# Kernel tuning notes

Hardware: AMD Instinct MI355X
Metric: run time of the kernel (lower is better)

The kernel has to match this reference:

```python
import jax, jax.numpy as jnp
import numpy as np

# Cleaned/faithful JAX port of TATLMPLayer. The original torch code has obvious
# typos (edge_type_feature_embedding used before assignment, self.weight_mlp vs
# self._weight_mlp, missing dim= in concatenate, elementwise mult of (B,E,K) with
# (K,D)); we implement the clearly intended math: two-level masked-softmax
# message passing over an incidence matrix H, gumbel-softmax typed edge
# embeddings, and a 4-head cross-attention to polyline features.

NEG_SLOPE = 0.01  # torch leaky_relu default
TAU = 0.5         # gumbel-softmax temperature 1/2


def _mlp(x, W1, b1, W2, b2):
    return jnp.maximum(x @ W1 + b1, 0.0) @ W2 + b2


def setup_inputs() -> dict:
    B, N, E, P, D, T, K, Hd = 2, 256, 512, 256, 128, 8, 8, 256
    key = jax.random.key(0)
    ks = jax.random.split(key, 40)
    g = lambda i, shape, s=0.05: jax.random.normal(ks[i], shape, dtype=jnp.float32) * s
    return {
        "agent_features": jax.random.normal(ks[0], (B, N, D), dtype=jnp.float32),
        "agent_types": jax.random.uniform(ks[1], (B, N, T), dtype=jnp.float32),
        "polyline_features": jax.random.normal(ks[2], (B, P, D), dtype=jnp.float32),
        "H": (jax.random.uniform(ks[3], (B, E, N)) < 0.1).astype(jnp.float32),
        "type_emb": g(4, (K, D)),
        "w_W1": g(5, (2 * D, Hd)), "w_b1": g(6, (Hd,)), "w_W2": g(7, (Hd, 1)), "w_b2": g(8, (1,)),
        "d_W1": g(9, (D + T, Hd)), "d_b1": g(10, (Hd,)), "d_W2": g(11, (Hd, K)), "d_b2": g(12, (K,)),
        "f_W1": g(13, (D + T, Hd)), "f_b1": g(14, (Hd,)), "f_W2": g(15, (Hd, 1)), "f_b2": g(16, (1,)),
        "o_W1": g(17, (4 * D, Hd)), "o_b1": g(18, (Hd,)), "o_W2": g(19, (Hd, D)), "o_b2": g(20, (D,)),
        "q_W": g(21, (3 * D, D)), "q_b": g(22, (D,)),
        "k_W": g(23, (D, D)), "k_b": g(24, (D,)),
        "v_W": g(25, (D, D)), "v_b": g(26, (D,)),
        "iq_W": g(27, (D, D)), "iq_b": g(28, (D,)),
        "ik_W": g(29, (D, D)), "ik_b": g(30, (D,)),
        "iv_W": g(31, (D, D)), "iv_b": g(32, (D,)),
        "op_W": g(33, (D, D)), "op_b": g(34, (D,)),
    }


def reference(agent_features, agent_types, polyline_features, H, type_emb,
              w_W1, w_b1, w_W2, w_b2, d_W1, d_b1, d_W2, d_b2,
              f_W1, f_b1, f_W2, f_b2, o_W1, o_b1, o_W2, o_b2,
              q_W, q_b, k_W, k_b, v_W, v_b,
              iq_W, iq_b, ik_W, ik_b, iv_W, iv_b, op_W, op_b):
    B, N, D = agent_features.shape
    E = H.shape[1]

    # level 1: incidence-aggregated edge features
    ef_init = jnp.einsum('ben,bnd->bed', H, agent_features)            # (B,E,D)
    pair = jnp.concatenate([
        jnp.broadcast_to(ef_init[:, :, None, :], (B, E, N, D)),
        jnp.broadcast_to(agent_features[:, None, :, :], (B, E, N, D))], axis=-1)
    ew = _mlp(pair, w_W1, w_b1, w_W2, w_b2)[..., 0]                    # (B,E,N)
    Hw = jax.nn.softmax(ew * H, axis=2) * H
    edge_features = jnp.einsum('ben,bnd->bed', Hw, agent_features)     # (B,E,D)

    # typed edge embedding via gumbel-softmax over edge types
    edge_type = jnp.einsum('ben,bnt->bet', H, agent_types)             # (B,E,T)
    et = jnp.concatenate([edge_features, edge_type], axis=-1)          # (B,E,D+T)
    logits = _mlp(et, d_W1, d_b1, d_W2, d_b2)                          # (B,E,K)
    u = jax.random.uniform(jax.random.key(42), logits.shape, minval=1e-6, maxval=1.0 - 1e-6)
    gumbel = -jnp.log(-jnp.log(u))
    distribution = jax.nn.softmax((logits + gumbel) / TAU, axis=-1)
    factor = jax.nn.sigmoid(_mlp(et, f_W1, f_b1, f_W2, f_b2))          # (B,E,1)
    edge_type_embedding = jnp.einsum('bek,kd->bed', factor * distribution, type_emb)

    # level 2: masked edge->agent message passing
    pair2 = jnp.concatenate([
        jnp.broadcast_to(edge_type_embedding[:, :, None, :], (B, E, N, D)),
        jnp.broadcast_to(agent_features[:, None, :, :], (B, E, N, D))], axis=-1)
    pair2 = pair2 * H[..., None]
    hw2 = jnp.where(_mlp(pair2, w_W1, w_b1, w_W2, w_b2)[..., 0] > 0,
                    _mlp(pair2, w_W1, w_b1, w_W2, w_b2)[..., 0], 0.0)
    # leaky relu (single-eval form)
    raw2 = _mlp(pair2, w_W1, w_b1, w_W2, w_b2)[..., 0]
    hw2 = jnp.where(raw2 > 0, raw2, NEG_SLOPE * raw2)                  # (B,E,N)
    Hw2 = jax.nn.softmax(hw2, axis=2) * H
    msg = jnp.einsum('ben,bef->bnf', Hw2,
                     jnp.concatenate([edge_features, edge_type_embedding], axis=-1))
    agent_feat = jnp.concatenate([msg, agent_features], axis=-1)       # (B,N,3D)

    # cross-attention to polylines (4 heads)
    Q = agent_feat @ q_W + q_b
    Kp = polyline_features @ k_W + k_b
    Vp = polyline_features @ v_W + v_b
    q2 = Q @ iq_W + iq_b
    k2 = Kp @ ik_W + ik_b
    v2 = Vp @ iv_W + iv_b
    nh, hd = 4, D // 4
    qh = q2.reshape(B, N, nh, hd)
    kh = k2.reshape(B, -1, nh, hd)
    vh = v2.reshape(B, -1, nh, hd)
    att = jax.nn.softmax(jnp.einsum('bqhd,bkhd->bhqk', qh, kh) / jnp.sqrt(jnp.float32(hd)), axis=-1)
    o = jnp.einsum('bhqk,bkhd->bqhd', att, vh).reshape(B, N, D)
    polyline_new = o @ op_W + op_b                                     # (B,N,D)

    agent_new = _mlp(jnp.concatenate([agent_feat, polyline_new], axis=-1),
                     o_W1, o_b1, o_W2, o_b2)                           # (B,N,D)
    return agent_new, polyline_new
```

## Files before the change

kernel.cpp:

```cpp
#include <hip/hip_runtime.h>
#include <math.h>

#define BB 2
#define NN 256
#define EE 512
#define PP 256
#define DD 128
#define TT 8
#define KK 8
#define HDIM 256

#define WS_G      0
#define WS_C0     8192
#define WS_V      8256
#define WS_EDGEF  139328
#define WS_ETE    270400
#define WS_HWT    401472
#define WS_K2     663616
#define WS_V2     729152

#define PB_GUM 16
#define PB_V   272
#define PB_END 528

__device__ inline unsigned rotl32(unsigned x, int d){ return (x<<d)|(x>>(32-d)); }

__device__ inline float bits_to_gumbel(unsigned bits){
  float f = __uint_as_float((bits>>9)|0x3f800000u) - 1.0f;
  const float minv = 1e-6f;
  const float maxv = 1.0f - 1e-6f;
  float u = f*(maxv-minv) + minv;
  u = fmaxf(minv, u);
  return -logf(-logf(u));
}

__device__ __forceinline__ void f4fma(float4& a, float x, const float4& w){
  a.x += x*w.x; a.y += x*w.y; a.z += x*w.z; a.w += x*w.w;
}

__device__ __forceinline__ void block_reduce2_max(float v[2], float* wred){
  int lane = threadIdx.x & 63, wid = threadIdx.x >> 6;
  #pragma unroll
  for (int s=32;s>0;s>>=1){
    #pragma unroll
    for (int r=0;r<2;r++){ float o = __shfl_xor(v[r], s, 64); v[r] = fmaxf(v[r],o); }
  }
  if (lane==0){
    #pragma unroll
    for (int r=0;r<2;r++) wred[wid*2+r]=v[r];
  }
  __syncthreads();
  #pragma unroll
  for (int r=0;r<2;r++)
    v[r] = fmaxf(fmaxf(wred[0*2+r],wred[1*2+r]), fmaxf(wred[2*2+r],wred[3*2+r]));
  __syncthreads();
}

__device__ __forceinline__ void block_reduce2_sum(float v[2], float* wred){
  int lane = threadIdx.x & 63, wid = threadIdx.x >> 6;
  #pragma unroll
  for (int s=32;s>0;s>>=1){
    #pragma unroll
    for (int r=0;r<2;r++){ v[r] += __shfl_xor(v[r], s, 64); }
  }
  if (lane==0){
    #pragma unroll
    for (int r=0;r<2;r++) wred[wid*2+r]=v[r];
  }
  __syncthreads();
  #pragma unroll
  for (int r=0;r<2;r++)
    v[r] = (wred[0*2+r]+wred[1*2+r]) + (wred[2*2+r]+wred[3*2+r]);
  __syncthreads();
}

__device__ __forceinline__ void mlp128_lds2(const float (*in)[DD], const float* W, const float* bias,
                                            float (*outl)[DD], float* part, int t){
  int c=(t&31)*4, ks=t>>5;
  float4 a[2];
  #pragma unroll
  for (int r=0;r<2;r++) a[r]=make_float4(0.f,0.f,0.f,0.f);
  #pragma unroll 4
  for (int i=ks*16;i<ks*16+16;i++){
    float4 w = *(const float4*)&W[(size_t)i*DD+c];
    #pragma unroll
    for (int r=0;r<2;r++) f4fma(a[r], in[r][i], w);
  }
  #pragma unroll
  for (int r=0;r<2;r++) *(float4*)&part[(ks*2+r)*DD+c]=a[r];
  __syncthreads();
  int cc=t&127, r=t>>7;
  {
    float s=0.f;
    #pragma unroll
    for (int k2=0;k2<8;k2++) s+=part[(k2*2+r)*DD+cc];
    outl[r][cc]=s+bias[cc];
  }
  __syncthreads();
}

__device__ __forceinline__ void mlp128_glob2(const float (*in)[DD], const float* W, const float* bias,
                                             float* dst, int r0, float* part, int t){
  int c=(t&31)*4, ks=t>>5;
  float4 a[2];
  #pragma unroll
  for (int r=0;r<2;r++) a[r]=make_float4(0.f,0.f,0.f,0.f);
  #pragma unroll 4
  for (int i=ks*16;i<ks*16+16;i++){
    float4 w = *(const float4*)&W[(size_t)i*DD+c];
    #pragma unroll
    for (int r=0;r<2;r++) f4fma(a[r], in[r][i], w);
  }
  #pragma unroll
  for (int r=0;r<2;r++) *(float4*)&part[(ks*2+r)*DD+c]=a[r];
  __syncthreads();
  int cc=t&127, r=t>>7;
  {
    float s=0.f;
    #pragma unroll
    for (int k2=0;k2<8;k2++) s+=part[(k2*2+r)*DD+cc];
    dst[(size_t)(r0+r)*DD+cc]=s+bias[cc];
  }
  __syncthreads();
}

__global__ void prep_kernel(float* g, float* c0, const float* w_b1,
                            const float* w_W2, const float* w_b2,
                            const float* af, const float* wW1, float* Vout,
                            const float* pf,
                            const float* kW, const float* kb, const float* ikW, const float* ikb,
                            const float* vW, const float* vb, const float* ivW, const float* ivb,
                            float* k2, float* v2){
  __shared__ float xs[2][DD];
  __shared__ float part[2048];
  __shared__ float wred[16];
  __shared__ float bufB[2][DD];
  int blk = blockIdx.x;
  int t = threadIdx.x;

  if (blk < PB_GUM){
    int j = blk*256 + t;
    {
      const unsigned k0=0u, k1=42u;
      const unsigned ks2 = k0^k1^0x1BD11BDAu;
      unsigned x0 = (unsigned)j, x1 = (unsigned)j + 4096u;
      const int r0_[4]={13,15,26,6}, r1_[4]={17,29,16,24};
      x0 += k0; x1 += k1;
      #pragma unroll
      for(int i=0;i<4;i++){ x0+=x1; x1=rotl32(x1,r0_[i]); x1^=x0; }
      x0+=k1; x1+=ks2+1u;
      #pragma unroll
      for(int i=0;i<4;i++){ x0+=x1; x1=rotl32(x1,r1_[i]); x1^=x0; }
      x0+=ks2; x1+=k0+2u;
      #pragma unroll
      for(int i=0;i<4;i++){ x0+=x1; x1=rotl32(x1,r0_[i]); x1^=x0; }
      x0+=k0; x1+=k1+3u;
      #pragma unroll
      for(int i=0;i<4;i++){ x0+=x1; x1=rotl32(x1,r1_[i]); x1^=x0; }
      x0+=k1; x1+=ks2+4u;
      #pragma unroll
      for(int i=0;i<4;i++){ x0+=x1; x1=rotl32(x1,r0_[i]); x1^=x0; }
      x0+=ks2; x1+=k0+5u;
      g[j]      = bits_to_gumbel(x0);
      g[j+4096] = bits_to_gumbel(x1);
    }
    if (blk == 0){
      float v4[2];
      v4[0] = fmaxf(w_b1[t],0.f)*w_W2[t]; v4[1]=0.f;
      block_reduce2_sum(v4, wred);
      if (t==0) c0[0] = v4[0] + w_b2[0];
    }
  } else if (blk < PB_V){
    int r0 = (blk - PB_GUM)*2;
    const float* W = wW1 + (size_t)DD*HDIM;
    for (int i=t;i<2*DD;i+=256) xs[i>>7][i&127] = af[(size_t)(r0+(i>>7))*DD + (i&127)];
    __syncthreads();
    int c = (t&63)*4, ks = t>>6;
    float4 acc[2];
    #pragma unroll
    for (int r=0;r<2;r++) acc[r]=make_float4(0.f,0.f,0.f,0.f);
    #pragma unroll 8
    for (int i=ks*32; i<ks*32+32; i++){
      float4 w = *(const float4*)&W[(size_t)i*HDIM + c];
      #pragma unroll
      for (int r=0;r<2;r++) f4fma(acc[r], xs[r][i], w);
    }
    #pragma unroll
    for (int r=0;r<2;r++) *(float4*)&part[(ks*2+r)*HDIM + c] = acc[r];
    __syncthreads();
    #pragma unroll
    for (int r=0;r<2;r++){
      float s = (part[(0*2+r)*HDIM+t] + part[(1*2+r)*HDIM+t])
              + (part[(2*2+r)*HDIM+t] + part[(3*2+r)*HDIM+t]);
      Vout[(size_t)(r0+r)*HDIM + t] = s;
    }
  } else {
    int r0 = (blk - PB_V)*2;
    for (int i=t;i<2*DD;i+=256) xs[i>>7][i&127] = pf[(size_t)(r0+(i>>7))*DD + (i&127)];
    __syncthreads();
    mlp128_lds2 (xs, kW, kb, bufB, part, t);
    mlp128_glob2(bufB, ikW, ikb, k2, r0, part, t);
    mlp128_lds2 (xs, vW, vb, bufB, part, t);
    mlp128_glob2(bufB, ivW, ivb, v2, r0, part, t);
  }
}

__global__ void edge_kernel(const float* Hm, const float* af, const float* at,
                            const float* Vm,
                            const float* wW1, const float* wb1, const float* wW2, const float* wb2,
                            const float* dW1, const float* db1, const float* dW2, const float* db2,
                            const float* fW1, const float* fb1, const float* fW2, const float* fb2,
                            const float* type_emb, const float* g, const float* c0p,
                            float* edgef_g, float* ete_g, float* HwT){
  __shared__ float bufA[2048];
  __shared__ float bufB[2048];
  __shared__ float w2s[HDIM*KK];
  __shared__ float w2l[HDIM];
  __shared__ float et4[2][144];
  __shared__ float hd4[2][HDIM];
  __shared__ float redsm[256];
  __shared__ float wred[16];
  __shared__ float facs[2];
  __shared__ float zz[2][KK];
  __shared__ float pzs[2][KK];
  __shared__ float fdv[2][KK];
  __shared__ int   hcnt[2];
  float* u    = bufB;
  float* hwls = bufB + 512;
  int*   hcomp= (int*)(bufB + 1024);

  int e0 = blockIdx.x*2;
  int b  = e0 >> 9;
  int t  = threadIdx.x;
  int lane = t & 63, wid = t >> 6;

  w2l[t] = wW2[t];
  for (int i=t;i<HDIM*KK;i+=256) w2s[i] = dW2[i];

  if (wid < 2){
    int r = wid;
    const float* Hrow = Hm + (size_t)(e0+r)*NN;
    int base = 0;
    #pragma unroll
    for (int c4=0;c4<4;c4++){
      int n2 = c4*64 + lane;
      bool pred = (Hrow[n2] != 0.f);
      unsigned long long mask = __ballot(pred);
      int off = __popcll(mask & ((1ull<<lane)-1ull));
      if (pred) hcomp[r*256+base+off] = n2;
      base += __popcll(mask);
    }
    if (lane==0) hcnt[r] = base;
  }
  __syncthreads();
  {
    int d = t & 127, r = t >> 7;
    int tot = hcnt[r];
    float a = 0.f, a2 = 0.f;
    for (int i=0;i<tot;i++){
      int n2 = hcomp[r*256+i];
      a += af[((size_t)b*NN+n2)*DD + d];
      if (d < TT) a2 += at[((size_t)b*NN+n2)*TT + d];
    }
    et4[r][d] = a;
    if (d < TT) et4[r][DD+d] = a2;
  }
  __syncthreads();
  {
    int c=(t&63)*4, ks=t>>6;
    float4 acc[2];
    #pragma unroll
    for (int r=0;r<2;r++) acc[r]=make_float4(0.f,0.f,0.f,0.f);
    #pragma unroll 8
    for (int i=ks*32; i<ks*32+32; i++){
      float4 w = *(const float4*)&wW1[(size_t)i*HDIM + c];
      #pragma unroll
      for (int r=0;r<2;r++) f4fma(acc[r], et4[r][i], w);
    }
    #pragma unroll
    for (int r=0;r<2;r++) *(float4*)&bufA[(ks*2+r)*HDIM + c] = acc[r];
  }
  __syncthreads();
  {
    float bv = wb1[t];
    #pragma unroll
    for (int r=0;r<2;r++){
      float s = (bufA[(0*2+r)*HDIM+t] + bufA[(1*2+r)*HDIM+t])
              + (bufA[(2*2+r)*HDIM+t] + bufA[(3*2+r)*HDIM+t]);
      u[r*HDIM + t] = s + bv;
    }
  }
  __syncthreads();
  {
    int n = t;
    const float4* Vrow = (const float4*)(Vm + ((size_t)(b*NN)+n)*HDIM);
    float acc[2]={0.f,0.f};
    #pragma unroll 4
    for (int ii=0;ii<HDIM/4;ii++){
      float4 v = Vrow[ii];
      float w0=w2l[4*ii+0], w1=w2l[4*ii+1], wc=w2l[4*ii+2], w3=w2l[4*ii+3];
      #pragma unroll
      for (int r=0;r<2;r++){
        acc[r] += fmaxf(u[r*HDIM+4*ii+0]+v.x,0.f)*w0
                + fmaxf(u[r*HDIM+4*ii+1]+v.y,0.f)*w1
                + fmaxf(u[r*HDIM+4*ii+2]+v.z,0.f)*wc
                + fmaxf(u[r*HDIM+4*ii+3]+v.w,0.f)*w3;
      }
    }
    float b2v = wb2[0];
    float x[2], hv[2];
    #pragma unroll
    for (int r=0;r<2;r++){
      hv[r] = Hm[(size_t)(e0+r)*NN + n];
      x[r] = (hv[r]!=0.f) ? (acc[r]+b2v) : 0.f;
    }
    float m2[2]={x[0],x[1]};
    block_reduce2_max(m2, wred);
    float p2[2];
    #pragma unroll
    for (int r=0;r<2;r++) p2[r]=expf(x[r]-m2[r]);
    float s2[2]={p2[0],p2[1]};
    block_reduce2_sum(s2, wred);
    #pragma unroll
    for (int r=0;r<2;r++)
      hwls[r*NN+n] = (hv[r]!=0.f) ? p2[r]/s2[r] : 0.f;
  }
  __syncthreads();
  {
    int d = t & 127, r = t >> 7;
    int tot = hcnt[r];
    float a = 0.f;
    for (int i=0;i<tot;i++){
      int n2 = hcomp[r*256+i];
      a += hwls[r*NN+n2]*af[((size_t)b*NN+n2)*DD + d];
    }
    et4[r][d] = a;
    edgef_g[(size_t)(e0+r)*DD + d] = a;
  }
  __syncthreads();
  {
    int c=(t&63)*4, ks=t>>6;
    float4 ad4[2], af4[2];
    #pragma unroll
    for (int r=0;r<2;r++){ ad4[r]=make_float4(0.f,0.f,0.f,0.f); af4[r]=make_float4(0.f,0.f,0.f,0.f); }
    #pragma unroll 4
    for (int i=ks*34;i<ks*34+34;i++){
      float4 wd = *(const float4*)&dW1[(size_t)i*HDIM+c];
      float4 wf = *(const float4*)&fW1[(size_t)i*HDIM+c];
      #pragma unroll
      for (int r=0;r<2;r++){ float x=et4[r][i]; f4fma(ad4[r],x,wd); f4fma(af4[r],x,wf); }
    }
    #pragma unroll
    for (int r=0;r<2;r++){
      *(float4*)&bufA[(ks*2+r)*HDIM+c]=ad4[r];
      *(float4*)&bufB[(ks*2+r)*HDIM+c]=af4[r];
    }
  }
  __syncthreads();
  {
    float bd = db1[t];
    float bf = fb1[t], fw = fW2[t];
    float v2_[2];
    #pragma unroll
    for (int r=0;r<2;r++){
      float sd = (bufA[(0*2+r)*HDIM+t]+bufA[(1*2+r)*HDIM+t])
               + (bufA[(2*2+r)*HDIM+t]+bufA[(3*2+r)*HDIM+t]);
      hd4[r][t] = fmaxf(sd+bd, 0.f);
      float sf = (bufB[(0*2+r)*HDIM+t]+bufB[(1*2+r)*HDIM+t])
               + (bufB[(2*2+r)*HDIM+t]+bufB[(3*2+r)*HDIM+t]);
      v2_[r] = fmaxf(sf+bf,0.f)*fw;
    }
    block_reduce2_sum(v2_, wred);
    if (t<2) facs[t] = 1.f/(1.f+expf(-(v2_[t]+fb2[0])));
  }
  {
    int r_ = t>>7, jj_ = (t>>3)&15, kk_ = t&7;
    float lp = 0.f;
    #pragma unroll 4
    for (int i=0;i<16;i++){
      int h = jj_ + 16*i;
      lp += hd4[r_][h]*w2s[h*KK + kk_];
    }
    redsm[t] = lp;
  }
  __syncthreads();
  if (t < 16){
    int r = t>>3, k = t&7;
    float s = db2[k] + g[(size_t)(e0+r)*KK + k];
    #pragma unroll
    for (int j=0;j<16;j++) s += redsm[(r<<7)|(j<<3)|k];
    zz[r][k] = s*2.0f;
  }
  __syncthreads();
  if (t < 16){
    int r = t>>3, k = t&7;
    float m = zz[r][0];
    #pragma unroll
    for (int k2=1;k2<KK;k2++) m = fmaxf(m, zz[r][k2]);
    pzs[r][k] = expf(zz[r][k]-m);
  }
  __syncthreads();
  if (t < 16){
    int r = t>>3, k = t&7;
    float s = 0.f;
    #pragma unroll
    for (int k2=0;k2<KK;k2++) s += pzs[r][k2];
    fdv[r][k] = facs[r]*pzs[r][k]/s;
  }
  __syncthreads();
  {
    int d = t&127, r = t>>7;
    float a = 0.f;
    #pragma unroll
    for (int k=0;k<KK;k++) a += fdv[r][k]*type_emb[(size_t)k*DD + d];
    et4[r][d] = a;
    ete_g[(size_t)(e0+r)*DD + d] = a;
  }
  __syncthreads();
  {
    int c=(t&63)*4, ks=t>>6;
    float4 a[2];
    #pragma unroll
    for (int r=0;r<2;r++) a[r]=make_float4(0.f,0.f,0.f,0.f);
    #pragma unroll 8
    for (int i=ks*32;i<ks*32+32;i++){
      float4 w = *(const float4*)&wW1[(size_t)i*HDIM+c];
      #pragma unroll
      for (int r=0;r<2;r++) f4fma(a[r], et4[r][i], w);
    }
    #pragma unroll
    for (int r=0;r<2;r++) *(float4*)&bufA[(ks*2+r)*HDIM+c]=a[r];
  }
  __syncthreads();
  {
    float bv = wb1[t];
    #pragma unroll
    for (int r=0;r<2;r++){
      float s = (bufA[(0*2+r)*HDIM+t]+bufA[(1*2+r)*HDIM+t])
              + (bufA[(2*2+r)*HDIM+t]+bufA[(3*2+r)*HDIM+t]);
      hd4[r][t] = s + bv;
    }
  }
  __syncthreads();
  {
    int n = t;
    const float4* Vrow = (const float4*)(Vm + ((size_t)(b*NN)+n)*HDIM);
    float acc[2]={0.f,0.f};
    #pragma unroll 4
    for (int ii=0;ii<HDIM/4;ii++){
      float4 v = Vrow[ii];
      float w0=w2l[4*ii+0], w1=w2l[4*ii+1], wc=w2l[4*ii+2], w3=w2l[4*ii+3];
      #pragma unroll
      for (int r=0;r<2;r++){
        acc[r] += fmaxf(hd4[r][4*ii+0]+v.x,0.f)*w0
                + fmaxf(hd4[r][4*ii+1]+v.y,0.f)*w1
                + fmaxf(hd4[r][4*ii+2]+v.z,0.f)*wc
                + fmaxf(hd4[r][4*ii+3]+v.w,0.f)*w3;
      }
    }
    float b2v = wb2[0];
    float c0 = c0p[0];
    float x[2], hv[2];
    #pragma unroll
    for (int r=0;r<2;r++){
      hv[r] = Hm[(size_t)(e0+r)*NN + n];
      float raw = (hv[r]!=0.f) ? (acc[r]+b2v) : c0;
      x[r] = raw>0.f ? raw : 0.01f*raw;
    }
    float m2[2]={x[0],x[1]};
    block_reduce2_max(m2, wred);
    float p2[2];
    #pragma unroll
    for (int r=0;r<2;r++) p2[r]=expf(x[r]-m2[r]);
    float s2[2]={p2[0],p2[1]};
    block_reduce2_sum(s2, wred);
    int eb = e0 & 511;
    float2 o2;
    o2.x = (hv[0]!=0.f)? p2[0]/s2[0] : 0.f;
    o2.y = (hv[1]!=0.f)? p2[1]/s2[1] : 0.f;
    *(float2*)(HwT + ((size_t)(b*NN)+n)*EE + eb) = o2;
  }
}

__global__ void agent_kernel(const float* HwT, const float* edgef, const float* ete,
                             const float* af,
                             const float* qW, const float* qb, const float* iqW, const float* iqb,
                             const float* k2, const float* v2,
                             const float* op_W, const float* op_b,
                             const float* oW1, const float* ob1,
                             const float* oW2, const float* ob2,
                             float* pnew, float* anew){
  __shared__ int   ecomp[EE];
  __shared__ float wcomp[EE];
  __shared__ int   wcnt[4];
  __shared__ float agfl[512];
  __shared__ float part[1024];
  __shared__ float Qs[DD];
  __shared__ float qr[DD];
  __shared__ float att[4][PP+1];
  __shared__ float o_l[DD];
  __shared__ float hid[HDIM];
  int bn = blockIdx.x; int b = bn >> 8; int t = threadIdx.x;
  int lane = t & 63, wid = t >> 6;

  {
    const float* wrow = HwT + (size_t)bn*EE;
    int total = 0;
    #pragma unroll
    for (int p=0;p<2;p++){
      int e = p*256 + t;
      float w = wrow[e];
      bool pred = (w != 0.f);
      unsigned long long mask = __ballot(pred);
      if (lane==0) wcnt[wid] = __popcll(mask);
      int off = __popcll(mask & ((1ull<<lane)-1ull));
      __syncthreads();
      int wb = total;
      for (int ww=0; ww<wid; ww++) wb += wcnt[ww];
      if (pred){ ecomp[wb+off] = e; wcomp[wb+off] = w; }
      total += wcnt[0]+wcnt[1]+wcnt[2]+wcnt[3];
      __syncthreads();
    }
    float acc = 0.f;
    const float* srcbase = (t < DD) ? (edgef + (size_t)b*EE*DD + t)
                                    : (ete   + (size_t)b*EE*DD + (t-DD));
    for (int i=0;i<total;i++){
      acc += wcomp[i] * srcbase[(size_t)ecomp[i]*DD];
    }
    agfl[t] = acc;
    if (t < DD) agfl[2*DD+t] = af[(size_t)bn*DD + t];
  }
  __syncthreads();
  int c=(t&31)*4, ps=t>>5;
  {
    float4 a = make_float4(0.f,0.f,0.f,0.f);
    #pragma unroll 4
    for (int i=ps*48;i<ps*48+48;i++){
      float4 w = *(const float4*)&qW[(size_t)i*DD+c];
      f4fma(a, agfl[i], w);
    }
    *(float4*)&part[ps*DD+c]=a;
  }
  __syncthreads();
  if (t<DD){
    float s=0.f;
    #pragma unroll
    for (int k=0;k<8;k++) s+=part[k*DD+t];
    Qs[t]=s+qb[t];
  }
  __syncthreads();
  {
    float4 a = make_float4(0.f,0.f,0.f,0.f);
    #pragma unroll 4
    for (int i=ps*16;i<ps*16+16;i++){
      float4 w = *(const float4*)&iqW[(size_t)i*DD+c];
      f4fma(a, Qs[i], w);
    }
    *(float4*)&part[ps*DD+c]=a;
  }
  __syncthreads();
  if (t<DD){
    float s=0.f;
    #pragma unroll
    for (int k=0;k<8;k++) s+=part[k*DD+t];
    qr[t]=s+iqb[t];
  }
  __syncthreads();
  const float scale = 0.17677669529663687f;
  const float* krow = k2 + ((size_t)(b*PP) + t)*DD;
  #pragma unroll
  for (int h=0;h<4;h++){
    const float4* k4 = (const float4*)(krow + h*32);
    float s = 0.f;
    #pragma unroll
    for (int jj=0;jj<8;jj++){
      float4 kk = k4[jj];
      s += qr[h*32+jj*4+0]*kk.x + qr[h*32+jj*4+1]*kk.y
         + qr[h*32+jj*4+2]*kk.z + qr[h*32+jj*4+3]*kk.w;
    }
    att[h][t] = s*scale;
  }
  __syncthreads();
  {
    int h = wid;
    float v0 = att[h][lane],     v1 = att[h][lane+64],
          ve = att[h][lane+128], v3 = att[h][lane+192];
    float m = fmaxf(fmaxf(v0,v1), fmaxf(ve,v3));
    #pragma unroll
    for (int s2=32;s2>0;s2>>=1) m = fmaxf(m, __shfl_xor(m, s2, 64));
    float e0 = expf(v0-m), e1 = expf(v1-m), e2 = expf(ve-m), e3 = expf(v3-m);
    float ss = (e0+e1)+(e2+e3);
    #pragma unroll
    for (int s2=32;s2>0;s2>>=1) ss += __shfl_xor(ss, s2, 64);
    float inv = 1.f/ss;
    att[h][lane] = e0*inv; att[h][lane+64] = e1*inv;
    att[h][lane+128] = e2*inv; att[h][lane+192] = e3*inv;
  }
  __syncthreads();
  int h2 = c >> 5;
  {
    float4 acc = make_float4(0.f,0.f,0.f,0.f);
    #pragma unroll 4
    for (int i=0;i<32;i++){
      int p = ps*32+i;
      float4 v = *(const float4*)&v2[((size_t)(b*PP)+p)*DD + c];
      f4fma(acc, att[h2][p], v);
    }
    *(float4*)&part[ps*DD+c]=acc;
  }
  __syncthreads();
  if (t<DD){
    float s=0.f;
    #pragma unroll
    for (int k=0;k<8;k++) s+=part[k*DD+t];
    o_l[t]=s;
  }
  __syncthreads();
  {
    float4 a2 = make_float4(0.f,0.f,0.f,0.f);
    #pragma unroll 4
    for (int i=ps*16;i<ps*16+16;i++){
      float4 w = *(const float4*)&op_W[(size_t)i*DD + c];
      f4fma(a2, o_l[i], w);
    }
    *(float4*)&part[ps*DD+c]=a2;
  }
  __syncthreads();
  if (t<DD){
    float s=0.f;
    #pragma unroll
    for (int k=0;k<8;k++) s+=part[k*DD+t];
    float pv = s+op_b[t];
    agfl[3*DD+t] = pv;
    pnew[(size_t)bn*DD+t] = pv;
  }
  __syncthreads();
  {
    int c1=(t&63)*4, ks1=t>>6;
    float4 acc = make_float4(0.f,0.f,0.f,0.f);
    #pragma unroll 8
    for (int i=ks1*128;i<ks1*128+128;i++){
      float4 w = *(const float4*)&oW1[(size_t)i*HDIM+c1];
      f4fma(acc, agfl[i], w);
    }
    *(float4*)&part[ks1*HDIM+c1]=acc;
  }
  __syncthreads();
  {
    float s = (part[0*HDIM+t]+part[1*HDIM+t]) + (part[2*HDIM+t]+part[3*HDIM+t]);
    hid[t] = fmaxf(s+ob1[t], 0.f);
  }
  __syncthreads();
  {
    float4 a2 = make_float4(0.f,0.f,0.f,0.f);
    #pragma unroll 8
    for (int h=ps*32;h<ps*32+32;h++){
      float4 w = *(const float4*)&oW2[(size_t)h*DD+c];
      f4fma(a2, hid[h], w);
    }
    *(float4*)&part[ps*DD+c]=a2;
  }
  __syncthreads();
  if (t<DD){
    float s=0.f;
    #pragma unroll
    for (int k=0;k<8;k++) s+=part[k*DD+t];
    anew[(size_t)bn*DD+t]=s+ob2[t];
  }
}

extern "C" void kernel_launch(void* const* d_in, const int* in_sizes, int n_in,
                              void* d_out, int out_size, void* d_ws, size_t ws_size,
                              hipStream_t stream) {
  const float* af       = (const float*)d_in[0];
  const float* at       = (const float*)d_in[1];
  const float* pf       = (const float*)d_in[2];
  const float* Hm       = (const float*)d_in[3];
  const float* type_emb = (const float*)d_in[4];
  const float* w_W1 = (const float*)d_in[5];
  const float* w_b1 = (const float*)d_in[6];
  const float* w_W2 = (const float*)d_in[7];
  const float* w_b2 = (const float*)d_in[8];
  const float* d_W1 = (const float*)d_in[9];
  const float* d_b1 = (const float*)d_in[10];
  const float* d_W2 = (const float*)d_in[11];
  const float* d_b2 = (const float*)d_in[12];
  const float* f_W1 = (const float*)d_in[13];
  const float* f_b1 = (const float*)d_in[14];
  const float* f_W2 = (const float*)d_in[15];
  const float* f_b2 = (const float*)d_in[16];
  const float* o_W1 = (const float*)d_in[17];
  const float* o_b1 = (const float*)d_in[18];
  const float* o_W2 = (const float*)d_in[19];
  const float* o_b2 = (const float*)d_in[20];
  const float* q_W  = (const float*)d_in[21];
  const float* q_b  = (const float*)d_in[22];
  const float* k_W  = (const float*)d_in[23];
  const float* k_b  = (const float*)d_in[24];
  const float* v_W  = (const float*)d_in[25];
  const float* v_b  = (const float*)d_in[26];
  const float* iq_W = (const float*)d_in[27];
  const float* iq_b = (const float*)d_in[28];
  const float* ik_W = (const float*)d_in[29];
  const float* ik_b = (const float*)d_in[30];
  const float* iv_W = (const float*)d_in[31];
  const float* iv_b = (const float*)d_in[32];
  const float* op_W = (const float*)d_in[33];
  const float* op_b = (const float*)d_in[34];

  float* ws   = (float*)d_ws;
  float* out  = (float*)d_out;
  float* anew = out;
  float* pnew = out + BB*NN*DD;

  prep_kernel<<<PB_END, 256, 0, stream>>>(
      ws+WS_G, ws+WS_C0, w_b1, w_W2, w_b2,
      af, w_W1, ws+WS_V,
      pf, k_W,k_b,ik_W,ik_b, v_W,v_b,iv_W,iv_b,
      ws+WS_K2, ws+WS_V2);
  edge_kernel<<<512,256,0,stream>>>(
      Hm, af, at, ws+WS_V,
      w_W1, w_b1, w_W2, w_b2,
      d_W1,d_b1,d_W2,d_b2, f_W1,f_b1,f_W2,f_b2,
      type_emb, ws+WS_G, ws+WS_C0,
      ws+WS_EDGEF, ws+WS_ETE, ws+WS_HWT);
  agent_kernel<<<BB*NN,256,0,stream>>>(
      ws+WS_HWT, ws+WS_EDGEF, ws+WS_ETE, af,
      q_W, q_b, iq_W, iq_b,
      ws+WS_K2, ws+WS_V2, op_W, op_b,
      o_W1,o_b1,o_W2,o_b2, pnew, anew);
}
```

Before: 101.2 us.

## Process four edges per block with 512 threads in edge kernel

Restructures edge_kernel so each block handles four hyperedges with 512 threads instead of two edges with 256 threads. The weight matrices wW1, dW1 and fW1 and the V rows are then reused across four edges per load, and the work is split across more waves per block. The softmax reductions become per-wave row reductions, and HwT is written as float4. The cost is more shared memory per block and half as many blocks (256) on the GPU, which may lower occupancy or leave CUs idle.

```diff
diff --git a/kernel.cpp b/kernel.cpp
--- a/kernel.cpp
+++ b/kernel.cpp
@@ -36,24 +36,6 @@
 
 __device__ __forceinline__ void f4fma(float4& a, float x, const float4& w){
   a.x += x*w.x; a.y += x*w.y; a.z += x*w.z; a.w += x*w.w;
-}
-
-__device__ __forceinline__ void block_reduce2_max(float v[2], float* wred){
-  int lane = threadIdx.x & 63, wid = threadIdx.x >> 6;
-  #pragma unroll
-  for (int s=32;s>0;s>>=1){
-    #pragma unroll
-    for (int r=0;r<2;r++){ float o = __shfl_xor(v[r], s, 64); v[r] = fmaxf(v[r],o); }
-  }
-  if (lane==0){
-    #pragma unroll
-    for (int r=0;r<2;r++) wred[wid*2+r]=v[r];
-  }
-  __syncthreads();
-  #pragma unroll
-  for (int r=0;r<2;r++)
-    v[r] = fmaxf(fmaxf(wred[0*2+r],wred[1*2+r]), fmaxf(wred[2*2+r],wred[3*2+r]));
-  __syncthreads();
 }
 
 __device__ __forceinline__ void block_reduce2_sum(float v[2], float* wred){
@@ -205,39 +187,38 @@
   }
 }
 
-__global__ void edge_kernel(const float* Hm, const float* af, const float* at,
+__global__ __launch_bounds__(512) void edge_kernel(
+                            const float* Hm, const float* af, const float* at,
                             const float* Vm,
                             const float* wW1, const float* wb1, const float* wW2, const float* wb2,
                             const float* dW1, const float* db1, const float* dW2, const float* db2,
                             const float* fW1, const float* fb1, const float* fW2, const float* fb2,
                             const float* type_emb, const float* g, const float* c0p,
                             float* edgef_g, float* ete_g, float* HwT){
-  __shared__ float bufA[2048];
-  __shared__ float bufB[2048];
+  __shared__ float bufA[8192];
   __shared__ float w2s[HDIM*KK];
   __shared__ float w2l[HDIM];
-  __shared__ float et4[2][144];
-  __shared__ float hd4[2][HDIM];
-  __shared__ float redsm[256];
+  __shared__ float et4[4][144];
+  __shared__ float hd4[4][HDIM];
+  __shared__ float redsm[512];
   __shared__ float wred[16];
-  __shared__ float facs[2];
-  __shared__ float zz[2][KK];
-  __shared__ float pzs[2][KK];
-  __shared__ float fdv[2][KK];
-  __shared__ int   hcnt[2];
-  float* u    = bufB;
-  float* hwls = bufB + 512;
-  int*   hcomp= (int*)(bufB + 1024);
-
-  int e0 = blockIdx.x*2;
+  __shared__ float mred[4], sinv[4];
+  __shared__ float facs[4];
+  __shared__ float zz[4][KK];
+  __shared__ float pzs[4][KK];
+  __shared__ float fdv[4][KK];
+  __shared__ int   hcnt[4];
+  __shared__ int   hcomp[4*256];
+
+  int e0 = blockIdx.x*4;
   int b  = e0 >> 9;
   int t  = threadIdx.x;
   int lane = t & 63, wid = t >> 6;
 
-  w2l[t] = wW2[t];
-  for (int i=t;i<HDIM*KK;i+=256) w2s[i] = dW2[i];
-
-  if (wid < 2){
+  if (t < HDIM) w2l[t] = wW2[t];
+  for (int i=t;i<HDIM*KK;i+=512) w2s[i] = dW2[i];
+
+  if (wid < 4){
     int r = wid;
     const float* Hrow = Hm + (size_t)(e0+r)*NN;
     int base = 0;
@@ -268,62 +249,86 @@
   __syncthreads();
   {
     int c=(t&63)*4, ks=t>>6;
-    float4 acc[2];
-    #pragma unroll
-    for (int r=0;r<2;r++) acc[r]=make_float4(0.f,0.f,0.f,0.f);
-    #pragma unroll 8
-    for (int i=ks*32; i<ks*32+32; i++){
+    float4 acc[4];
+    #pragma unroll
+    for (int r=0;r<4;r++) acc[r]=make_float4(0.f,0.f,0.f,0.f);
+    #pragma unroll 4
+    for (int i=ks*16; i<ks*16+16; i++){
       float4 w = *(const float4*)&wW1[(size_t)i*HDIM + c];
       #pragma unroll
-      for (int r=0;r<2;r++) f4fma(acc[r], et4[r][i], w);
-    }
-    #pragma unroll
-    for (int r=0;r<2;r++) *(float4*)&bufA[(ks*2+r)*HDIM + c] = acc[r];
-  }
-  __syncthreads();
-  {
-    float bv = wb1[t];
-    #pragma unroll
-    for (int r=0;r<2;r++){
-      float s = (bufA[(0*2+r)*HDIM+t] + bufA[(1*2+r)*HDIM+t])
-              + (bufA[(2*2+r)*HDIM+t] + bufA[(3*2+r)*HDIM+t]);
-      u[r*HDIM + t] = s + bv;
-    }
-  }
-  __syncthreads();
-  {
-    int n = t;
+      for (int r=0;r<4;r++) f4fma(acc[r], et4[r][i], w);
+    }
+    #pragma unroll
+    for (int r=0;r<4;r++) *(float4*)&bufA[(ks*4+r)*HDIM + c] = acc[r];
+  }
+  __syncthreads();
+  {
+    int h=t&255, rh=t>>8;
+    float bv = wb1[h];
+    #pragma unroll
+    for (int rr=0;rr<2;rr++){
+      int r = 2*rh+rr;
+      float s=0.f;
+      #pragma unroll
+      for (int k=0;k<8;k++) s += bufA[(k*4+r)*HDIM + h];
+      hd4[r][h] = s + bv;
+    }
+  }
+  __syncthreads();
+  {
+    int n = t&255, hh = t>>8;
     const float4* Vrow = (const float4*)(Vm + ((size_t)(b*NN)+n)*HDIM);
-    float acc[2]={0.f,0.f};
-    #pragma unroll 4
-    for (int ii=0;ii<HDIM/4;ii++){
+    float acc[4]={0.f,0.f,0.f,0.f};
+    #pragma unroll 4
+    for (int ii=hh*32; ii<hh*32+32; ii++){
       float4 v = Vrow[ii];
       float w0=w2l[4*ii+0], w1=w2l[4*ii+1], wc=w2l[4*ii+2], w3=w2l[4*ii+3];
       #pragma unroll
-      for (int r=0;r<2;r++){
-        acc[r] += fmaxf(u[r*HDIM+4*ii+0]+v.x,0.f)*w0
-                + fmaxf(u[r*HDIM+4*ii+1]+v.y,0.f)*w1
-                + fmaxf(u[r*HDIM+4*ii+2]+v.z,0.f)*wc
-                + fmaxf(u[r*HDIM+4*ii+3]+v.w,0.f)*w3;
+      for (int r=0;r<4;r++){
+        acc[r] += fmaxf(hd4[r][4*ii+0]+v.x,0.f)*w0
+                + fmaxf(hd4[r][4*ii+1]+v.y,0.f)*w1
+                + fmaxf(hd4[r][4*ii+2]+v.z,0.f)*wc
+                + fmaxf(hd4[r][4*ii+3]+v.w,0.f)*w3;
       }
     }
+    #pragma unroll
+    for (int r=0;r<4;r++) bufA[(hh*4+r)*256 + n] = acc[r];
+  }
+  __syncthreads();
+  {
+    int n = t&255, rh = t>>8;
     float b2v = wb2[0];
-    float x[2], hv[2];
-    #pragma unroll
-    for (int r=0;r<2;r++){
-      hv[r] = Hm[(size_t)(e0+r)*NN + n];
-      x[r] = (hv[r]!=0.f) ? (acc[r]+b2v) : 0.f;
-    }
-    float m2[2]={x[0],x[1]};
-    block_reduce2_max(m2, wred);
-    float p2[2];
-    #pragma unroll
-    for (int r=0;r<2;r++) p2[r]=expf(x[r]-m2[r]);
-    float s2[2]={p2[0],p2[1]};
-    block_reduce2_sum(s2, wred);
-    #pragma unroll
-    for (int r=0;r<2;r++)
-      hwls[r*NN+n] = (hv[r]!=0.f) ? p2[r]/s2[r] : 0.f;
+    #pragma unroll
+    for (int rr=0;rr<2;rr++){
+      int r = 2*rh+rr;
+      float hv = Hm[(size_t)(e0+r)*NN + n];
+      float xv = (hv!=0.f) ? (bufA[(0*4+r)*256+n] + bufA[(1*4+r)*256+n] + b2v) : 0.f;
+      bufA[2048 + r*256 + n] = xv;
+    }
+  }
+  __syncthreads();
+  if (wid < 4){
+    int r = wid;
+    float v0=bufA[2048+r*256+lane],     v1=bufA[2048+r*256+lane+64],
+          v2=bufA[2048+r*256+lane+128], v3=bufA[2048+r*256+lane+192];
+    float m = fmaxf(fmaxf(v0,v1), fmaxf(v2,v3));
+    #pragma unroll
+    for (int s2=32;s2>0;s2>>=1) m = fmaxf(m, __shfl_xor(m, s2, 64));
+    float ss = (expf(v0-m)+expf(v1-m)) + (expf(v2-m)+expf(v3-m));
+    #pragma unroll
+    for (int s2=32;s2>0;s2>>=1) ss += __shfl_xor(ss, s2, 64);
+    if (lane==0){ mred[r]=m; sinv[r]=1.f/ss; }
+  }
+  __syncthreads();
+  {
+    int n = t&255, rh = t>>8;
+    #pragma unroll
+    for (int rr=0;rr<2;rr++){
+      int r = 2*rh+rr;
+      float hv = Hm[(size_t)(e0+r)*NN + n];
+      float p = expf(bufA[2048+r*256+n] - mred[r]) * sinv[r];
+      bufA[3072 + r*256 + n] = (hv!=0.f) ? p : 0.f;
+    }
   }
   __syncthreads();
   {
@@ -332,67 +337,79 @@
     float a = 0.f;
     for (int i=0;i<tot;i++){
       int n2 = hcomp[r*256+i];
-      a += hwls[r*NN+n2]*af[((size_t)b*NN+n2)*DD + d];
+      a += bufA[3072 + r*256 + n2] * af[((size_t)b*NN+n2)*DD + d];
     }
     et4[r][d] = a;
     edgef_g[(size_t)(e0+r)*DD + d] = a;
   }
   __syncthreads();
   {
-    int c=(t&63)*4, ks=t>>6;
-    float4 ad4[2], af4[2];
-    #pragma unroll
-    for (int r=0;r<2;r++){ ad4[r]=make_float4(0.f,0.f,0.f,0.f); af4[r]=make_float4(0.f,0.f,0.f,0.f); }
+    int half = t>>8, tt = t&255;
+    int c=(tt&63)*4, ks=tt>>6;
+    const float* W = half ? fW1 : dW1;
+    float4 acc[4];
+    #pragma unroll
+    for (int r=0;r<4;r++) acc[r]=make_float4(0.f,0.f,0.f,0.f);
     #pragma unroll 4
     for (int i=ks*34;i<ks*34+34;i++){
-      float4 wd = *(const float4*)&dW1[(size_t)i*HDIM+c];
-      float4 wf = *(const float4*)&fW1[(size_t)i*HDIM+c];
-      #pragma unroll
-      for (int r=0;r<2;r++){ float x=et4[r][i]; f4fma(ad4[r],x,wd); f4fma(af4[r],x,wf); }
-    }
-    #pragma unroll
-    for (int r=0;r<2;r++){
-      *(float4*)&bufA[(ks*2+r)*HDIM+c]=ad4[r];
-      *(float4*)&bufB[(ks*2+r)*HDIM+c]=af4[r];
-    }
-  }
-  __syncthreads();
-  {
-    float bd = db1[t];
-    float bf = fb1[t], fw = fW2[t];
-    float v2_[2];
-    #pragma unroll
-    for (int r=0;r<2;r++){
-      float sd = (bufA[(0*2+r)*HDIM+t]+bufA[(1*2+r)*HDIM+t])
-               + (bufA[(2*2+r)*HDIM+t]+bufA[(3*2+r)*HDIM+t]);
-      hd4[r][t] = fmaxf(sd+bd, 0.f);
-      float sf = (bufB[(0*2+r)*HDIM+t]+bufB[(1*2+r)*HDIM+t])
-               + (bufB[(2*2+r)*HDIM+t]+bufB[(3*2+r)*HDIM+t]);
-      v2_[r] = fmaxf(sf+bf,0.f)*fw;
-    }
-    block_reduce2_sum(v2_, wred);
-    if (t<2) facs[t] = 1.f/(1.f+expf(-(v2_[t]+fb2[0])));
-  }
-  {
-    int r_ = t>>7, jj_ = (t>>3)&15, kk_ = t&7;
+      float4 w = *(const float4*)&W[(size_t)i*HDIM+c];
+      #pragma unroll
+      for (int r=0;r<4;r++) f4fma(acc[r], et4[r][i], w);
+    }
+    #pragma unroll
+    for (int r=0;r<4;r++) *(float4*)&bufA[half*4096 + (ks*4+r)*HDIM + c] = acc[r];
+  }
+  __syncthreads();
+  {
+    int h=t&255, rh=t>>8;
+    float bd = db1[h], bf = fb1[h], fw = fW2[h];
+    float val[2];
+    #pragma unroll
+    for (int rr=0;rr<2;rr++){
+      int r = 2*rh+rr;
+      float sd=0.f, sf=0.f;
+      #pragma unroll
+      for (int k=0;k<4;k++){ sd += bufA[(k*4+r)*HDIM+h]; sf += bufA[4096+(k*4+r)*HDIM+h]; }
+      hd4[r][h] = fmaxf(sd+bd, 0.f);
+      val[rr] = fmaxf(sf+bf, 0.f)*fw;
+    }
+    #pragma unroll
+    for (int s2=32;s2>0;s2>>=1){
+      val[0] += __shfl_xor(val[0], s2, 64);
+      val[1] += __shfl_xor(val[1], s2, 64);
+    }
+    if (lane==0){ wred[wid*2]=val[0]; wred[wid*2+1]=val[1]; }
+  }
+  __syncthreads();
+  if (t<4){
+    int r=t;
+    int base = (r>=2)?4:0, off = r&1;
+    float s = 0.f;
+    #pragma unroll
+    for (int w=0;w<4;w++) s += wred[(base+w)*2 + off];
+    facs[r] = 1.f/(1.f+expf(-(s+fb2[0])));
+  }
+  __syncthreads();
+  {
+    int r_ = t>>7, rem = t&127, k_ = rem&7, j_ = rem>>3;
     float lp = 0.f;
     #pragma unroll 4
     for (int i=0;i<16;i++){
-      int h = jj_ + 16*i;
-      lp += hd4[r_][h]*w2s[h*KK + kk_];
+      int h = j_ + 16*i;
+      lp += hd4[r_][h]*w2s[h*KK + k_];
     }
     redsm[t] = lp;
   }
   __syncthreads();
-  if (t < 16){
+  if (t < 32){
     int r = t>>3, k = t&7;
     float s = db2[k] + g[(size_t)(e0+r)*KK + k];
     #pragma unroll
-    for (int j=0;j<16;j++) s += redsm[(r<<7)|(j<<3)|k];
+    for (int j=0;j<16;j++) s += redsm[r*128 + j*8 + k];
     zz[r][k] = s*2.0f;
   }
   __syncthreads();
-  if (t < 16){
+  if (t < 32){
     int r = t>>3, k = t&7;
     float m = zz[r][0];
     #pragma unroll
@@ -400,7 +417,7 @@
     pzs[r][k] = expf(zz[r][k]-m);
   }
   __syncthreads();
-  if (t < 16){
+  if (t < 32){
     int r = t>>3, k = t&7;
     float s = 0.f;
     #pragma unroll
@@ -419,66 +436,90 @@
   __syncthreads();
   {
     int c=(t&63)*4, ks=t>>6;
-    float4 a[2];
-    #pragma unroll
-    for (int r=0;r<2;r++) a[r]=make_float4(0.f,0.f,0.f,0.f);
-    #pragma unroll 8
-    for (int i=ks*32;i<ks*32+32;i++){
-      float4 w = *(const float4*)&wW1[(size_t)i*HDIM+c];
-      #pragma unroll
-      for (int r=0;r<2;r++) f4fma(a[r], et4[r][i], w);
-    }
-    #pragma unroll
-    for (int r=0;r<2;r++) *(float4*)&bufA[(ks*2+r)*HDIM+c]=a[r];
-  }
-  __syncthreads();
-  {
-    float bv = wb1[t];
-    #pragma unroll
-    for (int r=0;r<2;r++){
-      float s = (bufA[(0*2+r)*HDIM+t]+bufA[(1*2+r)*HDIM+t])
-              + (bufA[(2*2+r)*HDIM+t]+bufA[(3*2+r)*HDIM+t]);
-      hd4[r][t] = s + bv;
-    }
-  }
-  __syncthreads();
-  {
-    int n = t;
+    float4 acc[4];
+    #pragma unroll
+    for (int r=0;r<4;r++) acc[r]=make_float4(0.f,0.f,0.f,0.f);
+    #pragma unroll 4
+    for (int i=ks*16; i<ks*16+16; i++){
+      float4 w = *(const float4*)&wW1[(size_t)i*HDIM + c];
+      #pragma unroll
+      for (int r=0;r<4;r++) f4fma(acc[r], et4[r][i], w);
+    }
+    #pragma unroll
+    for (int r=0;r<4;r++) *(float4*)&bufA[(ks*4+r)*HDIM + c] = acc[r];
+  }
+  __syncthreads();
+  {
+    int h=t&255, rh=t>>8;
+    float bv = wb1[h];
+    #pragma unroll
+    for (int rr=0;rr<2;rr++){
+      int r = 2*rh+rr;
+      float s=0.f;
+      #pragma unroll
+      for (int k=0;k<8;k++) s += bufA[(k*4+r)*HDIM + h];
+      hd4[r][h] = s + bv;
+    }
+  }
+  __syncthreads();
+  {
+    int n = t&255, hh = t>>8;
     const float4* Vrow = (const float4*)(Vm + ((size_t)(b*NN)+n)*HDIM);
-    float acc[2]={0.f,0.f};
-    #pragma unroll 4
-    for (int ii=0;ii<HDIM/4;ii++){
+    float acc[4]={0.f,0.f,0.f,0.f};
+    #pragma unroll 4
+    for (int ii=hh*32; ii<hh*32+32; ii++){
       float4 v = Vrow[ii];
       float w0=w2l[4*ii+0], w1=w2l[4*ii+1], wc=w2l[4*ii+2], w3=w2l[4*ii+3];
       #pragma unroll
-      for (int r=0;r<2;r++){
+      for (int r=0;r<4;r++){
         acc[r] += fmaxf(hd4[r][4*ii+0]+v.x,0.f)*w0
                 + fmaxf(hd4[r][4*ii+1]+v.y,0.f)*w1
                 + fmaxf(hd4[r][4*ii+2]+v.z,0.f)*wc
                 + fmaxf(hd4[r][4*ii+3]+v.w,0.f)*w3;
       }
     }
+    #pragma unroll
+    for (int r=0;r<4;r++) bufA[(hh*4+r)*256 + n] = acc[r];
+  }
+  __syncthreads();
+  {
+    int n = t&255, rh = t>>8;
     float b2v = wb2[0];
     float c0 = c0p[0];
-    float x[2], hv[2];
-    #pragma unroll
-    for (int r=0;r<2;r++){
-      hv[r] = Hm[(size_t)(e0+r)*NN + n];
-      float raw = (hv[r]!=0.f) ? (acc[r]+b2v) : c0;
-      x[r] = raw>0.f ? raw : 0.01f*raw;
-    }
-    float m2[2]={x[0],x[1]};
-    block_reduce2_max(m2, wred);
-    float p2[2];
-    #pragma unroll
-    for (int r=0;r<2;r++) p2[r]=expf(x[r]-m2[r]);
-    float s2[2]={p2[0],p2[1]};
-    block_reduce2_sum(s2, wred);
+    #pragma unroll
+    for (int rr=0;rr<2;rr++){
+      int r = 2*rh+rr;
+      float hv = Hm[(size_t)(e0+r)*NN + n];
+      float raw = (hv!=0.f) ? (bufA[(0*4+r)*256+n] + bufA[(1*4+r)*256+n] + b2v) : c0;
+      bufA[2048 + r*256 + n] = raw>0.f ? raw : 0.01f*raw;
+    }
+  }
+  __syncthreads();
+  if (wid < 4){
+    int r = wid;
+    float v0=bufA[2048+r*256+lane],     v1=bufA[2048+r*256+lane+64],
+          v2=bufA[2048+r*256+lane+128], v3=bufA[2048+r*256+lane+192];
+    float m = fmaxf(fmaxf(v0,v1), fmaxf(v2,v3));
+    #pragma unroll
+    for (int s2=32;s2>0;s2>>=1) m = fmaxf(m, __shfl_xor(m, s2, 64));
+    float ss = (expf(v0-m)+expf(v1-m)) + (expf(v2-m)+expf(v3-m));
+    #pragma unroll
+    for (int s2=32;s2>0;s2>>=1) ss += __shfl_xor(ss, s2, 64);
+    if (lane==0){ mred[r]=m; sinv[r]=1.f/ss; }
+  }
+  __syncthreads();
+  if (t < 256){
+    int n = t;
+    float o[4];
+    #pragma unroll
+    for (int r=0;r<4;r++){
+      float hv = Hm[(size_t)(e0+r)*NN + n];
+      float p = expf(bufA[2048+r*256+n] - mred[r]) * sinv[r];
+      o[r] = (hv!=0.f) ? p : 0.f;
+    }
     int eb = e0 & 511;
-    float2 o2;
-    o2.x = (hv[0]!=0.f)? p2[0]/s2[0] : 0.f;
-    o2.y = (hv[1]!=0.f)? p2[1]/s2[1] : 0.f;
-    *(float2*)(HwT + ((size_t)(b*NN)+n)*EE + eb) = o2;
+    float4 o4; o4.x=o[0]; o4.y=o[1]; o4.z=o[2]; o4.w=o[3];
+    *(float4*)(HwT + ((size_t)(b*NN)+n)*EE + eb) = o4;
   }
 }
 
@@ -718,7 +759,7 @@
       af, w_W1, ws+WS_V,
       pf, k_W,k_b,ik_W,ik_b, v_W,v_b,iv_W,iv_b,
       ws+WS_K2, ws+WS_V2);
-  edge_kernel<<<512,256,0,stream>>>(
+  edge_kernel<<<256,512,0,stream>>>(
       Hm, af, at, ws+WS_V,
       w_W1, w_b1, w_W2, w_b2,
       d_W1,d_b1,d_W2,d_b2, f_W1,f_b1,f_W2,f_b2,
```

Measured after the change: 90.60 us. -10.5%, faster.
